# Kernel tuning notes

Hardware: AMD Instinct MI355X
Metric: run time of the kernel (lower is better)

## Reference

```python
import jax, jax.numpy as jnp
import numpy as np

LATENT_DIM = 128
NUM_QUANTIZERS = 8
CODEBOOK_SIZE = 1024


def setup_inputs() -> dict:
    key = jax.random.key(0)
    k1, k2 = jax.random.split(key)
    z = jax.random.normal(k1, (8, LATENT_DIM, 4096), dtype=jnp.float32)
    scale = 1.0 / np.sqrt(LATENT_DIM)
    codebooks = jax.random.uniform(
        k2, (NUM_QUANTIZERS, CODEBOOK_SIZE, LATENT_DIM),
        minval=-scale, maxval=scale, dtype=jnp.float32)
    return {"z": z, "codebooks": codebooks}


def _nearest_indices(x_flat, codebook):
    # x_flat: [N, D], codebook: [K, D] -> [N] argmin of squared L2 distance
    d = (jnp.sum(x_flat * x_flat, axis=1, keepdims=True)
         - 2.0 * x_flat @ codebook.T
         + jnp.sum(codebook * codebook, axis=1)[None, :])
    return jnp.argmin(d, axis=1)


def reference(z, codebooks):
    # z: [B, D, S] -> z_bsd: [B, S, D]
    z_bsd = jnp.transpose(z, (0, 2, 1))
    B, S, D = z_bsd.shape
    Q, K, _ = codebooks.shape

    residual = z_bsd
    quantized = jnp.zeros_like(z_bsd)
    idx_list = []
    for q in range(Q):  # small fixed loop over quantizer stages
        cb = codebooks[q]
        idx = _nearest_indices(residual.reshape(-1, D), cb).reshape(B, S)
        selected = cb[idx]                       # [B, S, D] gather
        quantized = quantized + selected
        residual = residual - jax.lax.stop_gradient(selected)
        idx_list.append(idx)
    indices = jnp.stack(idx_list, axis=-1)        # [B, S, Q]

    commitment_loss = jnp.mean(
        (z_bsd - jax.lax.stop_gradient(quantized)) ** 2)
    quantized_st = z_bsd + jax.lax.stop_gradient(quantized - z_bsd)

    def _perplexity(ix):  # ix: [B, S] codes for one quantizer
        counts = jnp.zeros((K,), jnp.float32).at[ix.reshape(-1)].add(1.0)
        probs = counts / jnp.maximum(counts.sum(), 1.0)
        entropy = -jnp.sum(probs * jnp.log(probs + 1e-10))
        return jnp.exp(entropy)

    perplexity = jnp.mean(jax.vmap(_perplexity, in_axes=2)(indices))

    return (jnp.transpose(quantized_st, (0, 2, 1)),  # [B, D, S]
            indices, commitment_loss, perplexity)
```

## Files before the change

kernel.cpp:

```cpp
#include <hip/hip_runtime.h>
#include <math.h>
#include <stdint.h>

#define D       128
#define KCODES  1024
#define NQ      8
#define BATCH   8
#define SLEN    4096
#define NPTS    (BATCH*SLEN)
#define TM      64

typedef __attribute__((address_space(1))) const void GV;
typedef __attribute__((address_space(3))) void LV;
__device__ __forceinline__ void gload16(const void* g, void* l) {
    __builtin_amdgcn_global_load_lds((GV*)g, (LV*)l, 16, 0, 0);
}

__global__ void k_zero(int* hist, double* csum) {
    int t = blockIdx.x * blockDim.x + threadIdx.x;
    if (t < NQ * KCODES) hist[t] = 0;
    if (t == 0) *csum = 0.0;
}

__global__ void k_c2(const float* __restrict__ cbs, float* __restrict__ c2f) {
    int i = blockIdx.x * blockDim.x + threadIdx.x;
    const float* row = cbs + (size_t)i * D;
    float r8[8];
    #pragma unroll
    for (int j = 0; j < 8; ++j) r8[j] = __fmul_rn(row[j], row[j]);
    for (int d = 8; d < 128; d += 8)
        #pragma unroll
        for (int j = 0; j < 8; ++j)
            r8[j] = __fadd_rn(r8[j], __fmul_rn(row[d + j], row[d + j]));
    float s01 = __fadd_rn(r8[0], r8[1]);
    float s23 = __fadd_rn(r8[2], r8[3]);
    float s45 = __fadd_rn(r8[4], r8[5]);
    float s67 = __fadd_rn(r8[6], r8[7]);
    c2f[i] = __fadd_rn(__fadd_rn(s01, s23), __fadd_rn(s45, s67));
}

__global__ __launch_bounds__(256) void k_init(const float* __restrict__ z,
                                              float* __restrict__ resid,
                                              float* __restrict__ quant) {
    __shared__ float xt[64][129];
    int b = blockIdx.x >> 6, st = blockIdx.x & 63;
    int s0 = st * 64;
    for (int it = 0; it < 32; ++it) {
        int flat = it * 256 + threadIdx.x;
        int d = flat >> 6, sl = flat & 63;
        xt[sl][d] = z[((size_t)(b * D + d)) * SLEN + s0 + sl];
    }
    __syncthreads();
    for (int it = 0; it < 8; ++it) {
        int flat = it * 256 + threadIdx.x;
        int sl = flat >> 5, dq = (flat & 31) * 4;
        size_t o = (size_t)(b * SLEN + s0 + sl) * D + dq;
        float4 r;
        r.x = xt[sl][dq]; r.y = xt[sl][dq + 1];
        r.z = xt[sl][dq + 2]; r.w = xt[sl][dq + 3];
        *(float4*)(resid + o) = r;
        float4 zz; zz.x = zz.y = zz.z = zz.w = 0.0f;
        *(float4*)(quant + o) = zz;
    }
}

__global__ __launch_bounds__(256) void k_argmin(const float* __restrict__ cb,
                                                const float* __restrict__ c2,
                                                const float* __restrict__ resid,
                                                int* __restrict__ idx_out) {
    __shared__ __align__(16) float xs[TM][132];
    __shared__ float xxs[TM];
    __shared__ __align__(16) float cs[4][2][128][8];
    __shared__ __align__(16) float ccl[4][256];
    __shared__ float redS[4][TM];
    __shared__ int   redI[4][TM];

    int tid = threadIdx.x;
    int pbase = blockIdx.x * TM;
    int l = tid & 63, w = tid >> 6;
    int pl = l & 7, cl = l >> 3;

    const char* cwb = (const char*)cb + ((size_t)w << 17);
    int gsrc_lane = ((l >> 1) << 9) + ((l & 1) << 4);
    char* csw = (char*)&cs[w][0][0][0];
    const char* xsb = (const char*)&xs[0][0];

    {
        const char* src = cwb + gsrc_lane;
        gload16(src,             csw);
        gload16(src + (1 << 14), csw + 1024);
        gload16(src + (2 << 14), csw + 2048);
        gload16(src + (3 << 14), csw + 3072);
    }
    {
        float4 cv = *(const float4*)(c2 + (w << 8) + l * 4);
        *(float4*)&ccl[w][l * 4] = cv;
    }

    #pragma unroll
    for (int it = 0; it < 8; ++it) {
        int e = (it * 256 + tid) * 4;
        int p = e >> 7, d = e & 127;
        *(float4*)&xs[p][d] = *(const float4*)(resid + (size_t)(pbase + p) * D + d);
    }
    __syncthreads();

    if (tid < TM) {
        float r8[8];
        #pragma unroll
        for (int j = 0; j < 8; ++j) r8[j] = __fmul_rn(xs[tid][j], xs[tid][j]);
        for (int i = 8; i < 128; i += 8)
            #pragma unroll
            for (int j = 0; j < 8; ++j)
                r8[j] = __fadd_rn(r8[j], __fmul_rn(xs[tid][i + j], xs[tid][i + j]));
        float s01 = __fadd_rn(r8[0], r8[1]);
        float s23 = __fadd_rn(r8[2], r8[3]);
        float s45 = __fadd_rn(r8[4], r8[5]);
        float s67 = __fadd_rn(r8[6], r8[7]);
        xxs[tid] = __fadd_rn(__fadd_rn(s01, s23), __fadd_rn(s45, s67));
    }
    __syncthreads();

    float xxr[8];
    #pragma unroll
    for (int i = 0; i < 8; ++i) xxr[i] = xxs[pl + 8 * i];

    float acc[8][16];
    #pragma unroll
    for (int i = 0; i < 8; ++i)
        #pragma unroll
        for (int j = 0; j < 16; ++j) acc[i][j] = 0.0f;
    float best[8]; int bidx[8];
    #pragma unroll
    for (int i = 0; i < 8; ++i) { best[i] = 3.4e38f; bidx[i] = 0; }

    #pragma unroll 1
    for (int t = 0; t < 32; ++t) {
        int c = t >> 4, s = t & 15, buf = t & 1;
        if (t < 31) {
            int t2 = t + 1;
            const char* src = cwb + gsrc_lane + ((t2 >> 4) << 16) + ((t2 & 15) << 5);
            char* dst = csw + ((t2 & 1) << 12);
            gload16(src,             dst);
            gload16(src + (1 << 14), dst + 1024);
            gload16(src + (2 << 14), dst + 2048);
            gload16(src + (3 << 14), dst + 3072);
            asm volatile("s_waitcnt vmcnt(4)" ::: "memory");
        } else {
            asm volatile("s_waitcnt vmcnt(0)" ::: "memory");
        }
        const char* cbuf = csw + (buf << 12) + (cl << 5);
        const char* xrow = xsb + pl * 528 + (s << 5);
        #pragma unroll
        for (int d4 = 0; d4 < 2; ++d4) {
            float4 xf[8];
            #pragma unroll
            for (int i = 0; i < 8; ++i)
                xf[i] = *(const float4*)(xrow + i * 4224 + (d4 << 4));
            #pragma unroll
            for (int jb = 0; jb < 4; ++jb) {
                float4 cf[4];
                #pragma unroll
                for (int j = 0; j < 4; ++j)
                    cf[j] = *(const float4*)(cbuf + ((jb * 4 + j) << 8) + (d4 << 4));
                #pragma unroll
                for (int j = 0; j < 4; ++j) {
                    int jj = jb * 4 + j;
                    #pragma unroll
                    for (int i = 0; i < 8; ++i) {
                        acc[i][jj] = __fmaf_rn(xf[i].x, cf[j].x, acc[i][jj]);
                        acc[i][jj] = __fmaf_rn(xf[i].y, cf[j].y, acc[i][jj]);
                        acc[i][jj] = __fmaf_rn(xf[i].z, cf[j].z, acc[i][jj]);
                        acc[i][jj] = __fmaf_rn(xf[i].w, cf[j].w, acc[i][jj]);
                    }
                }
            }
        }
        if (s == 15) {
            #pragma unroll
            for (int j = 0; j < 16; ++j) {
                float cc = ccl[w][(c << 7) + cl + (j << 3)];
                int k = (w << 8) + (c << 7) + cl + (j << 3);
                #pragma unroll
                for (int i = 0; i < 8; ++i) {
                    float t1  = __fadd_rn(xxr[i], __fmul_rn(-2.0f, acc[i][j]));
                    float dsc = __fadd_rn(t1, cc);
                    if (dsc < best[i]) { best[i] = dsc; bidx[i] = k; }
                    acc[i][j] = 0.0f;
                }
            }
        }
    }

    #pragma unroll
    for (int i = 0; i < 8; ++i) {
        float b = best[i]; int bi = bidx[i];
        #pragma unroll
        for (int off = 8; off < 64; off <<= 1) {
            float b2 = __shfl_xor(b, off, 64);
            int  bi2 = __shfl_xor(bi, off, 64);
            if (b2 < b || (b2 == b && bi2 < bi)) { b = b2; bi = bi2; }
        }
        if (cl == 0) { redS[w][pl + 8 * i] = b; redI[w][pl + 8 * i] = bi; }
    }
    __syncthreads();
    if (tid < TM) {
        float b = redS[0][tid]; int bi = redI[0][tid];
        #pragma unroll
        for (int ww = 1; ww < 4; ++ww) {
            float b2 = redS[ww][tid]; int bi2 = redI[ww][tid];
            if (b2 < b || (b2 == b && bi2 < bi)) { b = b2; bi = bi2; }
        }
        idx_out[pbase + tid] = bi;
    }
}

__global__ void k_update(const float* __restrict__ cb, const int* __restrict__ idx,
                         float* __restrict__ resid, float* __restrict__ quant) {
    int gid = blockIdx.x * blockDim.x + threadIdx.x;
    int n = gid >> 5, d4 = (gid & 31) * 4;
    int k = idx[n];
    float4 c = *(const float4*)(cb + (size_t)k * D + d4);
    size_t o = (size_t)n * D + d4;
    float4 r = *(const float4*)(resid + o);
    float4 q = *(const float4*)(quant + o);
    r.x = __fsub_rn(r.x, c.x); r.y = __fsub_rn(r.y, c.y);
    r.z = __fsub_rn(r.z, c.z); r.w = __fsub_rn(r.w, c.w);
    q.x = __fadd_rn(q.x, c.x); q.y = __fadd_rn(q.y, c.y);
    q.z = __fadd_rn(q.z, c.z); q.w = __fadd_rn(q.w, c.w);
    *(float4*)(resid + o) = r;
    *(float4*)(quant + o) = q;
}

__global__ __launch_bounds__(256) void k_out0(const float* __restrict__ z,
                                              const float* __restrict__ quant,
                                              float* __restrict__ out0,
                                              double* __restrict__ csum) {
    __shared__ float xt[64][129];
    __shared__ double wsum[4];
    int b = blockIdx.x >> 6, st = blockIdx.x & 63;
    int s0 = st * 64;
    for (int it = 0; it < 8; ++it) {
        int flat = it * 256 + threadIdx.x;
        int sl = flat >> 5, dq = (flat & 31) * 4;
        float4 q = *(const float4*)(quant + (size_t)(b * SLEN + s0 + sl) * D + dq);
        xt[sl][dq] = q.x; xt[sl][dq + 1] = q.y;
        xt[sl][dq + 2] = q.z; xt[sl][dq + 3] = q.w;
    }
    __syncthreads();
    double v = 0.0;
    for (int it = 0; it < 32; ++it) {
        int flat = it * 256 + threadIdx.x;
        int d = flat >> 6, sl = flat & 63;
        size_t o = ((size_t)(b * D + d)) * SLEN + s0 + sl;
        float zz = z[o], qq = xt[sl][d];
        out0[o] = __fadd_rn(zz, __fsub_rn(qq, zz));
        float e = __fsub_rn(zz, qq);
        v += (double)e * (double)e;
    }
    for (int off = 32; off > 0; off >>= 1) v += __shfl_down(v, off, 64);
    int lane = threadIdx.x & 63, wv = threadIdx.x >> 6;
    if (lane == 0) wsum[wv] = v;
    __syncthreads();
    if (threadIdx.x == 0) {
        double tsum = wsum[0] + wsum[1] + wsum[2] + wsum[3];
        atomicAdd(csum, tsum);
    }
}

__global__ void k_outidx(const int* __restrict__ idx, float* __restrict__ out1) {
    int o = blockIdx.x * blockDim.x + threadIdx.x;
    int q = o & 7, n = o >> 3;
    out1[o] = (float)idx[q * NPTS + n];
}

__global__ void k_hist(const int* __restrict__ idx, int* __restrict__ hist) {
    int o = blockIdx.x * blockDim.x + threadIdx.x;
    int q = o >> 15;
    atomicAdd(&hist[q * KCODES + idx[o]], 1);
}

__global__ __launch_bounds__(256) void k_final(const int* __restrict__ hist,
                                               const double* __restrict__ csum,
                                               float* __restrict__ outs) {
    __shared__ double sh[256];
    double perp = 0.0;
    for (int q = 0; q < NQ; ++q) {
        double h = 0.0;
        for (int k = threadIdx.x; k < KCODES; k += 256) {
            double p = (double)hist[q * KCODES + k] / (double)NPTS;
            h -= p * log(p + 1e-10);
        }
        sh[threadIdx.x] = h; __syncthreads();
        for (int off = 128; off > 0; off >>= 1) {
            if (threadIdx.x < off) sh[threadIdx.x] += sh[threadIdx.x + off];
            __syncthreads();
        }
        if (threadIdx.x == 0) perp += exp(sh[0]);
        __syncthreads();
    }
    if (threadIdx.x == 0) {
        outs[0] = (float)(*csum / (double)((size_t)NPTS * D));
        outs[1] = (float)(perp / (double)NQ);
    }
}

extern "C" void kernel_launch(void* const* d_in, const int* in_sizes, int n_in,
                              void* d_out, int out_size, void* d_ws, size_t ws_size,
                              hipStream_t stream) {
    const float* z  = (const float*)d_in[0];
    const float* cb = (const float*)d_in[1];
    float* out0 = (float*)d_out;
    float* out1 = out0 + 4194304;
    float* outs = out1 + 262144;

    char* w = (char*)d_ws;
    float* resid  = (float*)w;
    float* quant  = (float*)(w + 16777216);
    int*   idx    = (int*)(w + 33554432);
    int*   hist   = (int*)(w + 34603008);
    double* csum  = (double*)(w + 34635776);
    float* c2f    = (float*)(w + 34635840);

    k_zero<<<32, 256, 0, stream>>>(hist, csum);
    k_c2<<<32, 256, 0, stream>>>(cb, c2f);
    k_init<<<512, 256, 0, stream>>>(z, resid, quant);

    for (int q = 0; q < NQ; ++q) {
        const float* cbq = cb + (size_t)q * KCODES * D;
        k_argmin<<<NPTS / TM, 256, 0, stream>>>(cbq, c2f + q * KCODES, resid,
                                                idx + q * NPTS);
        k_update<<<NPTS * 32 / 256, 256, 0, stream>>>(cbq, idx + q * NPTS,
                                                      resid, quant);
    }

    k_out0<<<512, 256, 0, stream>>>(z, quant, out0, csum);
    k_outidx<<<NPTS * NQ / 256, 256, 0, stream>>>(idx, out1);
    k_hist<<<NPTS * NQ / 256, 256, 0, stream>>>(idx, hist);
    k_final<<<1, 256, 0, stream>>>(hist, csum, outs);
}
```

Measured before the change: 1.177 ms.

## Split codebook search across two blocks per point tile and merge partial argmins

```diff
diff --git a/kernel.cpp b/kernel.cpp
--- a/kernel.cpp
+++ b/kernel.cpp
@@ -67,33 +67,34 @@
 __global__ __launch_bounds__(256) void k_argmin(const float* __restrict__ cb,
                                                 const float* __restrict__ c2,
                                                 const float* __restrict__ resid,
-                                                int* __restrict__ idx_out) {
+                                                float* __restrict__ pbest,
+                                                int* __restrict__ pidx) {
     __shared__ __align__(16) float xs[TM][132];
-    __shared__ float xxs[TM];
-    __shared__ __align__(16) float cs[4][2][128][8];
-    __shared__ __align__(16) float ccl[4][256];
+    __shared__ __align__(16) float cs[4][2][512];
+    __shared__ __align__(16) float ccl[4][128];
     __shared__ float redS[4][TM];
     __shared__ int   redI[4][TM];
 
     int tid = threadIdx.x;
-    int pbase = blockIdx.x * TM;
+    int u = blockIdx.x;
+    int pblk = u >> 1, half = u & 1;
+    int pbase = pblk * TM;
     int l = tid & 63, w = tid >> 6;
     int pl = l & 7, cl = l >> 3;
 
-    const char* cwb = (const char*)cb + ((size_t)w << 17);
-    int gsrc_lane = ((l >> 1) << 9) + ((l & 1) << 4);
-    char* csw = (char*)&cs[w][0][0][0];
+    const char* cwb = (const char*)cb + ((size_t)(half * 512 + w * 128) << 9);
+    char* csw = (char*)&cs[w][0][0];
     const char* xsb = (const char*)&xs[0][0];
 
-    {
-        const char* src = cwb + gsrc_lane;
-        gload16(src,             csw);
-        gload16(src + (1 << 14), csw + 1024);
-        gload16(src + (2 << 14), csw + 2048);
-        gload16(src + (3 << 14), csw + 3072);
-    }
-    {
-        float4 cv = *(const float4*)(c2 + (w << 8) + l * 4);
+#define ISSUE(S) { \
+    const char* _src = cwb + ((size_t)l << 9) + ((S) << 4); \
+    char* _dst = csw + (((S) & 1) << 11); \
+    gload16(_src,             _dst); \
+    gload16(_src + (1 << 15), _dst + 1024); }
+
+    ISSUE(0);
+    if (l < 32) {
+        float4 cv = *(const float4*)(c2 + half * 512 + w * 128 + l * 4);
         *(float4*)&ccl[w][l * 4] = cv;
     }
 
@@ -117,13 +118,13 @@
         float s23 = __fadd_rn(r8[2], r8[3]);
         float s45 = __fadd_rn(r8[4], r8[5]);
         float s67 = __fadd_rn(r8[6], r8[7]);
-        xxs[tid] = __fadd_rn(__fadd_rn(s01, s23), __fadd_rn(s45, s67));
+        xs[tid][128] = __fadd_rn(__fadd_rn(s01, s23), __fadd_rn(s45, s67));
     }
     __syncthreads();
 
     float xxr[8];
     #pragma unroll
-    for (int i = 0; i < 8; ++i) xxr[i] = xxs[pl + 8 * i];
+    for (int i = 0; i < 8; ++i) xxr[i] = xs[pl + 8 * i][128];
 
     float acc[8][16];
     #pragma unroll
@@ -136,59 +137,47 @@
 
     #pragma unroll 1
     for (int t = 0; t < 32; ++t) {
-        int c = t >> 4, s = t & 15, buf = t & 1;
         if (t < 31) {
-            int t2 = t + 1;
-            const char* src = cwb + gsrc_lane + ((t2 >> 4) << 16) + ((t2 & 15) << 5);
-            char* dst = csw + ((t2 & 1) << 12);
-            gload16(src,             dst);
-            gload16(src + (1 << 14), dst + 1024);
-            gload16(src + (2 << 14), dst + 2048);
-            gload16(src + (3 << 14), dst + 3072);
-            asm volatile("s_waitcnt vmcnt(4)" ::: "memory");
+            ISSUE(t + 1);
+            asm volatile("s_waitcnt vmcnt(2)" ::: "memory");
         } else {
             asm volatile("s_waitcnt vmcnt(0)" ::: "memory");
         }
-        const char* cbuf = csw + (buf << 12) + (cl << 5);
-        const char* xrow = xsb + pl * 528 + (s << 5);
-        #pragma unroll
-        for (int d4 = 0; d4 < 2; ++d4) {
-            float4 xf[8];
+        const char* cbuf = csw + ((t & 1) << 11) + (cl << 4);
+        const char* xrow = xsb + pl * 528 + (t << 4);
+        float4 xf[8];
+        #pragma unroll
+        for (int i = 0; i < 8; ++i)
+            xf[i] = *(const float4*)(xrow + i * 4224);
+        #pragma unroll
+        for (int jb = 0; jb < 4; ++jb) {
+            float4 cf[4];
             #pragma unroll
-            for (int i = 0; i < 8; ++i)
-                xf[i] = *(const float4*)(xrow + i * 4224 + (d4 << 4));
+            for (int j = 0; j < 4; ++j)
+                cf[j] = *(const float4*)(cbuf + ((jb * 4 + j) << 7));
             #pragma unroll
-            for (int jb = 0; jb < 4; ++jb) {
-                float4 cf[4];
+            for (int j = 0; j < 4; ++j) {
+                int jj = jb * 4 + j;
                 #pragma unroll
-                for (int j = 0; j < 4; ++j)
-                    cf[j] = *(const float4*)(cbuf + ((jb * 4 + j) << 8) + (d4 << 4));
-                #pragma unroll
-                for (int j = 0; j < 4; ++j) {
-                    int jj = jb * 4 + j;
-                    #pragma unroll
-                    for (int i = 0; i < 8; ++i) {
-                        acc[i][jj] = __fmaf_rn(xf[i].x, cf[j].x, acc[i][jj]);
-                        acc[i][jj] = __fmaf_rn(xf[i].y, cf[j].y, acc[i][jj]);
-                        acc[i][jj] = __fmaf_rn(xf[i].z, cf[j].z, acc[i][jj]);
-                        acc[i][jj] = __fmaf_rn(xf[i].w, cf[j].w, acc[i][jj]);
-                    }
+                for (int i = 0; i < 8; ++i) {
+                    acc[i][jj] = __fmaf_rn(xf[i].x, cf[j].x, acc[i][jj]);
+                    acc[i][jj] = __fmaf_rn(xf[i].y, cf[j].y, acc[i][jj]);
+                    acc[i][jj] = __fmaf_rn(xf[i].z, cf[j].z, acc[i][jj]);
+                    acc[i][jj] = __fmaf_rn(xf[i].w, cf[j].w, acc[i][jj]);
                 }
             }
         }
-        if (s == 15) {
-            #pragma unroll
-            for (int j = 0; j < 16; ++j) {
-                float cc = ccl[w][(c << 7) + cl + (j << 3)];
-                int k = (w << 8) + (c << 7) + cl + (j << 3);
-                #pragma unroll
-                for (int i = 0; i < 8; ++i) {
-                    float t1  = __fadd_rn(xxr[i], __fmul_rn(-2.0f, acc[i][j]));
-                    float dsc = __fadd_rn(t1, cc);
-                    if (dsc < best[i]) { best[i] = dsc; bidx[i] = k; }
-                    acc[i][j] = 0.0f;
-                }
-            }
+    }
+
+    #pragma unroll
+    for (int j = 0; j < 16; ++j) {
+        float cc = ccl[w][cl + (j << 3)];
+        int k = half * 512 + (w << 7) + cl + (j << 3);
+        #pragma unroll
+        for (int i = 0; i < 8; ++i) {
+            float t1  = __fadd_rn(xxr[i], __fmul_rn(-2.0f, acc[i][j]));
+            float dsc = __fadd_rn(t1, cc);
+            if (dsc < best[i]) { best[i] = dsc; bidx[i] = k; }
         }
     }
 
@@ -211,8 +200,18 @@
             float b2 = redS[ww][tid]; int bi2 = redI[ww][tid];
             if (b2 < b || (b2 == b && bi2 < bi)) { b = b2; bi = bi2; }
         }
-        idx_out[pbase + tid] = bi;
-    }
+        pbest[half * NPTS + pbase + tid] = b;
+        pidx [half * NPTS + pbase + tid] = bi;
+    }
+#undef ISSUE
+}
+
+__global__ void k_merge(const float* __restrict__ pbest, const int* __restrict__ pidx,
+                        int* __restrict__ idxq) {
+    int n = blockIdx.x * blockDim.x + threadIdx.x;
+    float a = pbest[n], b = pbest[NPTS + n];
+    int ia = pidx[n], ib = pidx[NPTS + n];
+    idxq[n] = (b < a) ? ib : ia;
 }
 
 __global__ void k_update(const float* __restrict__ cb, const int* __restrict__ idx,
@@ -321,6 +320,8 @@
     int*   hist   = (int*)(w + 34603008);
     double* csum  = (double*)(w + 34635776);
     float* c2f    = (float*)(w + 34635840);
+    float* pbest  = (float*)(w + 34668608);
+    int*   pidx   = (int*)(w + 34930752);
 
     k_zero<<<32, 256, 0, stream>>>(hist, csum);
     k_c2<<<32, 256, 0, stream>>>(cb, c2f);
@@ -328,8 +329,9 @@
 
     for (int q = 0; q < NQ; ++q) {
         const float* cbq = cb + (size_t)q * KCODES * D;
-        k_argmin<<<NPTS / TM, 256, 0, stream>>>(cbq, c2f + q * KCODES, resid,
-                                                idx + q * NPTS);
+        k_argmin<<<2 * NPTS / TM, 256, 0, stream>>>(cbq, c2f + q * KCODES, resid,
+                                                    pbest, pidx);
+        k_merge<<<NPTS / 256, 256, 0, stream>>>(pbest, pidx, idx + q * NPTS);
         k_update<<<NPTS * 32 / 256, 256, 0, stream>>>(cbq, idx + q * NPTS,
                                                       resid, quant);
     }
```

Result: no change. 1.168 ms (-0.8%).
